# Optimization experiments

Hardware: AMD Instinct MI355X
Metric: run time of the kernel (lower is better)

The kernel has to match this reference:

```python
import jax, jax.numpy as jnp
import numpy as np

EPS = 1e-06
K = 16  # instance ids 1..K
W_IOU, W_VAR, W_SEED = 1.0, 10.0, 1.0


def _lovasz_hinge_flat(logits, labels):
    # logits, labels: (N,) flat; labels in {0,1}
    signs = 2.0 * labels - 1.0
    errors = 1.0 - logits * signs
    perm = jnp.argsort(-errors)  # descending
    errors_sorted = errors[perm]
    gt_sorted = labels[perm]
    gts = gt_sorted.sum()
    intersection = gts - jnp.cumsum(gt_sorted)
    union = gts + jnp.cumsum(1.0 - gt_sorted)
    jaccard = 1.0 - intersection / jnp.maximum(union, 1e-08)
    jaccard = jnp.concatenate([jaccard[:1], jaccard[1:] - jaccard[:-1]])
    return jnp.dot(jax.nn.relu(errors_sorted), jaccard)


def _forward(y_pred, y_true):
    B, C, H, W = y_pred.shape
    D = 2
    off = y_pred[:, :D]              # (B,D,H,W)
    sig = y_pred[:, D:2 * D]         # (B,D,H,W)
    seed = y_pred[:, 2 * D]          # (B,H,W)
    dt = y_pred.dtype

    gy, gx = jnp.meshgrid(jnp.arange(H, dtype=dt), jnp.arange(W, dtype=dt), indexing='ij')
    grid = jnp.stack([gy, gx])       # (D,H,W)
    emb = grid[None] + off           # (B,D,H,W)

    ids = jnp.arange(1, K + 1)
    mask = (y_true[:, None] == ids[None, :, None, None]).astype(dt)  # (B,K,H,W)
    count = mask.sum((2, 3))                                         # (B,K)
    safe = jnp.maximum(count, 1.0)
    present = (count > 0).astype(dt)
    n_present = jnp.maximum(present.sum(), 1.0)

    # per-instance embedding centers
    Ck = jnp.einsum('bkhw,bdhw->bkd', mask, emb) / safe[..., None]   # (B,K,D)
    sb = jnp.maximum(sig, EPS)                                       # (B,D,H,W)
    diff = emb[:, None] - Ck[..., None, None]                        # (B,K,D,H,W)
    quad = diff * diff / (2.0 * sb[:, None] ** 2)
    phi = jnp.clip(jnp.exp(-quad.sum(2)), EPS, 1.0 - EPS)            # (B,K,H,W)
    logits = jnp.log(phi) - jnp.log1p(-phi)

    lov = jax.vmap(_lovasz_hinge_flat)(logits.reshape(B * K, -1), mask.reshape(B * K, -1))
    L_iou = (lov * present.reshape(-1)).sum() / n_present

    # sigma smoothness: mean over instances of mean_{d,pixels in mask}|sig - mean_k(sig)|
    mean_sig = jnp.einsum('bkhw,bdhw->bkd', mask, sig) / safe[..., None]  # (B,K,D)
    dev = (jnp.abs(sig[:, None] - mean_sig[..., None, None]) * mask[:, :, None]).sum((2, 3, 4))
    dev = dev / (D * safe)                                           # (B,K)
    L_var = (dev * present).sum() / n_present

    seed_target = (phi * mask).sum(1)                                # (B,H,W)
    L_seed = jnp.mean((seed - seed_target) ** 2)

    return W_IOU * L_iou + W_VAR * L_var + W_SEED * L_seed


def setup_inputs() -> dict:
    key = jax.random.key(0)
    k1, k2 = jax.random.split(key)
    B, H, W = 4, 768, 768
    y_pred = jax.random.uniform(k1, (B, 5, H, W), dtype=jnp.float32)
    y_true = jax.random.randint(k2, (B, H, W), 0, K + 1)
    return {"y_pred": y_pred, "y_true": y_true}


def reference(y_pred, y_true):
    return _forward(y_pred, y_true)
```

## Files before the change

### kernel.cpp

```cpp
#include <hip/hip_runtime.h>

#define HWPIX 589824
#define Wdim 768
#define Bdim 4
#define Kdim 16
#define NBINS 2048
#define RANGE_F 16.0f
#define BIN_W (RANGE_F / NBINS)
#define INV_BIN_W (NBINS / RANGE_F)
#define EPSf 1e-6f
#define QCLIP 13.8155106f

#define NSB 192
#define Q4 (HWPIX / 4)
#define GPI (NSB * 256)
#define NTHREADS_TOT (NSB * Bdim * 256)

#define ACC_OFF 0
#define CK_OFF 320
#define MSW_OFF 448
#define NPRES_OFF 720
#define LOVARR_OFF 724
#define HIST_OFF_F 1024
#define NHIST (Bdim * Kdim * 2 * NBINS)
#define POSNH_OFF_F (HIST_OFF_F + NHIST)
#define SPART_OFF (POSNH_OFF_F + 64)
#define MPART_OFF (SPART_OFF + Bdim * NSB * 80)

__global__ __launch_bounds__(256, 3) void k_stats(const float* __restrict__ yp,
                                                  const int* __restrict__ yt,
                                                  float* __restrict__ ws,
                                                  unsigned* __restrict__ hist) {
    int b = blockIdx.y;
    int lane = threadIdx.x & 63;
    int wv = threadIdx.x >> 6;
    __shared__ float lpart[4][80];

    {
        int gtid = (blockIdx.y * NSB + blockIdx.x) * 256 + threadIdx.x;
        for (int i = gtid; i < NHIST + 64; i += NTHREADS_TOT) hist[i] = 0u;
    }

    const float4* bp4 = (const float4*)(yp + (size_t)b * 5 * HWPIX);
    const int4* bt4 = (const int4*)(yt + (size_t)b * HWPIX);

    float acc[80];
#pragma unroll
    for (int v = 0; v < 80; ++v) acc[v] = 0.f;

    for (int p = 0; p < 3; ++p) {
        int g = p * GPI + blockIdx.x * 256 + threadIdx.x;
        float4 voy = bp4[g];
        float4 vox = bp4[g + Q4];
        float4 vsy = bp4[g + 2 * Q4];
        float4 vsx = bp4[g + 3 * Q4];
        int4 vt = bt4[g];
        int hwb = g * 4;
        float oy[4] = {voy.x, voy.y, voy.z, voy.w};
        float ox[4] = {vox.x, vox.y, vox.z, vox.w};
        float sy[4] = {vsy.x, vsy.y, vsy.z, vsy.w};
        float sx[4] = {vsx.x, vsx.y, vsx.z, vsx.w};
        int tt[4] = {vt.x, vt.y, vt.z, vt.w};
#pragma unroll
        for (int j = 0; j < 4; ++j) {
            int hw = hwb + j;
            int h = hw / Wdim;
            int w = hw - h * Wdim;
            int own = tt[j] - 1;
            float vy = (float)h + oy[j];
            float vx = (float)w + ox[j];
#pragma unroll
            for (int k = 0; k < Kdim; ++k) {
                float m = (own == k) ? 1.0f : 0.0f;
                acc[k * 5 + 0] += m;
                acc[k * 5 + 1] = fmaf(m, vy, acc[k * 5 + 1]);
                acc[k * 5 + 2] = fmaf(m, vx, acc[k * 5 + 2]);
                acc[k * 5 + 3] = fmaf(m, sy[j], acc[k * 5 + 3]);
                acc[k * 5 + 4] = fmaf(m, sx[j], acc[k * 5 + 4]);
            }
        }
    }

    bool lo = (lane < 32);
#pragma unroll
    for (int v = 0; v < 40; ++v) {
        float send = lo ? acc[v + 40] : acc[v];
        float got = __shfl_xor(send, 32);
        acc[v] += lo ? got : 0.f;
        acc[v + 40] += lo ? 0.f : got;
    }
#pragma unroll
    for (int v = 0; v < 40; ++v) {
        float x = lo ? acc[v] : acc[v + 40];
#pragma unroll
        for (int o = 16; o >= 1; o >>= 1) x += __shfl_xor(x, o);
        if ((lane & 31) == 0) lpart[wv][lo ? v : v + 40] = x;
    }
    __syncthreads();
    if (threadIdx.x < 80) {
        float v = lpart[0][threadIdx.x] + lpart[1][threadIdx.x] +
                  lpart[2][threadIdx.x] + lpart[3][threadIdx.x];
        ws[SPART_OFF + (size_t)(b * NSB + blockIdx.x) * 80 + threadIdx.x] = v;
    }
}

__global__ void k_centers(float* __restrict__ ws) {
    int t = threadIdx.x;
    int b = t / 80, idx = t - b * 80;
    float s = 0.f;
    const float* sp = ws + SPART_OFF + (size_t)b * NSB * 80 + idx;
    for (int j = 0; j < NSB; ++j) s += sp[j * 80];
    ws[ACC_OFF + t] = s;
    __syncthreads();
    if (t < 64) {
        float cnt = ws[ACC_OFF + t * 5];
        float safe = fmaxf(cnt, 1.0f);
        ws[CK_OFF + t * 2 + 0] = ws[ACC_OFF + t * 5 + 1] / safe;
        ws[CK_OFF + t * 2 + 1] = ws[ACC_OFF + t * 5 + 2] / safe;
        int bb = t >> 4, kk = t & 15;
        float* mw = ws + MSW_OFF + (size_t)(bb * 17 + kk) * 4;
        mw[0] = ws[ACC_OFF + t * 5 + 3] / safe;
        mw[1] = ws[ACC_OFF + t * 5 + 4] / safe;
        mw[2] = (cnt > 0.f) ? 0.5f / cnt : 0.f;
        mw[3] = 0.f;
    }
    if (t >= 64 && t < 68) {
        float* mw = ws + MSW_OFF + (size_t)((t - 64) * 17 + 16) * 4;
        mw[0] = mw[1] = mw[2] = mw[3] = 0.f;
    }
    __syncthreads();
    if (t == 0) {
        float s2 = 0.f;
        for (int j = 0; j < 64; ++j) s2 += (ws[ACC_OFF + j * 5] > 0.f) ? 1.f : 0.f;
        ws[NPRES_OFF] = fmaxf(s2, 1.0f);
    }
}

__global__ __launch_bounds__(256, 3) void k_main(const float* __restrict__ yp,
                                                 const int* __restrict__ yt,
                                                 float* __restrict__ ws,
                                                 unsigned* __restrict__ hist) {
    int b = blockIdx.y;
    int lane = threadIdx.x & 63;
    int wv = threadIdx.x >> 6;
    __shared__ float ck_s[32];
    __shared__ float4 msw_s[17];
    __shared__ float part[4][2];
    if (threadIdx.x < 32) ck_s[threadIdx.x] = ws[CK_OFF + b * 32 + threadIdx.x];
    if (threadIdx.x < 17)
        msw_s[threadIdx.x] = ((const float4*)(ws + MSW_OFF))[b * 17 + threadIdx.x];
    __syncthreads();

    float cky[Kdim], ckx[Kdim];
#pragma unroll
    for (int k = 0; k < Kdim; ++k) {
        cky[k] = ck_s[k * 2];
        ckx[k] = ck_s[k * 2 + 1];
    }

    unsigned* hb = hist + (size_t)(b * Kdim) * 2 * NBINS;
    unsigned* posnh = hist + (size_t)NHIST;
    const float4* bp4 = (const float4*)(yp + (size_t)b * 5 * HWPIX);
    const int4* bt4 = (const int4*)(yt + (size_t)b * HWPIX);

    float varsum = 0.f, ssum = 0.f;
    for (int p = 0; p < 3; ++p) {
        int g = p * GPI + blockIdx.x * 256 + threadIdx.x;
        float4 voy = bp4[g];
        float4 vox = bp4[g + Q4];
        float4 vsy = bp4[g + 2 * Q4];
        float4 vsx = bp4[g + 3 * Q4];
        float4 vse = bp4[g + 4 * Q4];
        int4 vt = bt4[g];
        int hwb = g * 4;
        float oy[4] = {voy.x, voy.y, voy.z, voy.w};
        float ox[4] = {vox.x, vox.y, vox.z, vox.w};
        float sya[4] = {vsy.x, vsy.y, vsy.z, vsy.w};
        float sxa[4] = {vsx.x, vsx.y, vsx.z, vsx.w};
        float sea[4] = {vse.x, vse.y, vse.z, vse.w};
        int tt[4] = {vt.x, vt.y, vt.z, vt.w};
#pragma unroll
        for (int j = 0; j < 4; ++j) {
            int hw = hwb + j;
            int h = hw / Wdim;
            int w = hw - h * Wdim;
            int own = tt[j] - 1;
            float sy = sya[j], sx = sxa[j];
            float ey = (float)h + oy[j], ex = (float)w + ox[j];
            float sby = fmaxf(sy, EPSf), sbx = fmaxf(sx, EPSf);
            float iy = 0.5f / (sby * sby), ix = 0.5f / (sbx * sbx);

            unsigned sm = 0;
#pragma unroll
            for (int k = 0; k < Kdim; ++k) {
                float dy = ey - cky[k];
                float dx = ex - ckx[k];
                float q = fmaf(dy * dy, iy, dx * dx * ix);
                if (q < QCLIP) sm |= (1u << k);
            }
            int ow = (own >= 0) ? own : 16;
            float4 mw = msw_s[ow];
            float devv = fabsf(sy - mw.x) + fabsf(sx - mw.y);
            varsum = fmaf(devv, mw.z, varsum);

            float st = (own >= 0) ? EPSf : 0.f;
            while (sm) {
                int k = __ffs(sm) - 1;
                sm &= sm - 1;
                float dy = ey - ck_s[k * 2];
                float dx = ex - ck_s[k * 2 + 1];
                float q = fmaf(dy * dy, iy, dx * dx * ix);
                float phi = expf(-q);
                phi = fminf(fmaxf(phi, EPSf), 1.0f - EPSf);
                float lg = logf(phi) - log1pf(-phi);
                bool isPos = (k == own);
                float e;
                if (isPos) {
                    st = phi;
                    atomicAdd(&posnh[b * Kdim + k], 1u);
                    e = 1.0f - lg;
                } else {
                    e = 1.0f + lg;
                }
                if (e > 0.f) {
                    int bin = (int)(e * INV_BIN_W);
                    if (bin > NBINS - 1) bin = NBINS - 1;
                    atomicAdd(&hb[(k * 2 + (isPos ? 1 : 0)) * NBINS + bin], 1u);
                }
            }
            float dd = sea[j] - st;
            ssum = fmaf(dd, dd, ssum);
        }
    }
#pragma unroll
    for (int o = 32; o >= 1; o >>= 1) {
        varsum += __shfl_xor(varsum, o);
        ssum += __shfl_xor(ssum, o);
    }
    if (lane == 0) {
        part[wv][0] = varsum;
        part[wv][1] = ssum;
    }
    __syncthreads();
    if (threadIdx.x < 2) {
        float v = part[0][threadIdx.x] + part[1][threadIdx.x] +
                  part[2][threadIdx.x] + part[3][threadIdx.x];
        ws[MPART_OFF + (size_t)(b * NSB + blockIdx.x) * 2 + threadIdx.x] = v;
    }
}

__global__ void k_lovasz(float* __restrict__ ws, const unsigned* __restrict__ hist) {
    int i = blockIdx.x;
    int lane = threadIdx.x;
    float P = ws[ACC_OFF + i * 5];
    if (P < 0.5f) {
        if (lane == 0) ws[LOVARR_OFF + i] = 0.f;
        return;
    }
    const unsigned* hn = hist + (size_t)i * 2 * NBINS;
    const unsigned* hp = hn + NBINS;
    const unsigned* posnh = hist + (size_t)NHIST;
    const float C_LO = logf(EPSf) - log1pf(-EPSf);
    const int HOTBIN = (int)((1.0f - C_LO) * INV_BIN_W);
    int deficit = (int)(P + 0.5f) - (int)posnh[i];
    int carry_p = 0, carry_n = 0;
    float Jtop = 0.f;
    float trap = 0.f;
    for (int c = NBINS / 64 - 1; c >= 0; --c) {
        int m = c * 64 + lane;
        int vp = (int)hp[m];
        int vn = (int)hn[m];
        if (m == HOTBIN) vp += deficit;
        for (int o = 1; o < 64; o <<= 1) {
            int tp = __shfl_down(vp, o);
            int tn = __shfl_down(vn, o);
            if (lane + o < 64) { vp += tp; vn += tn; }
        }
        float p_edge = (float)(carry_p + vp);
        float n_edge = (float)(carry_n + vn);
        float J = 1.0f - (P - p_edge) / (P + n_edge);
        float Jn = __shfl_down(J, 1);
        if (lane == 63) Jn = Jtop;
        trap += 0.5f * (J + Jn);
        carry_p += __shfl(vp, 0);
        carry_n += __shfl(vn, 0);
        Jtop = __shfl(J, 0);
    }
    for (int o = 1; o < 64; o <<= 1) {
        float t2 = __shfl_down(trap, o);
        if (lane + o < 64) trap += t2;
    }
    if (lane == 0) ws[LOVARR_OFF + i] = trap * BIN_W;
}

__global__ void k_final(const float* __restrict__ ws, float* __restrict__ out) {
    __shared__ float r0[256], r1[256], r2[256];
    int t = threadIdx.x;
    float v = 0.f, s = 0.f, l = 0.f;
    for (int j = t; j < Bdim * NSB; j += 256) {
        v += ws[MPART_OFF + 2 * j];
        s += ws[MPART_OFF + 2 * j + 1];
    }
    if (t < 64) l = ws[LOVARR_OFF + t];
    r0[t] = v; r1[t] = s; r2[t] = l;
    __syncthreads();
    for (int o = 128; o > 0; o >>= 1) {
        if (t < o) { r0[t] += r0[t + o]; r1[t] += r1[t + o]; r2[t] += r2[t + o]; }
        __syncthreads();
    }
    if (t == 0) {
        float npres = ws[NPRES_OFF];
        out[0] = r2[0] / npres + 10.0f * (r0[0] / npres) +
                 r1[0] / (float)((size_t)Bdim * HWPIX);
    }
}

extern "C" void kernel_launch(void* const* d_in, const int* in_sizes, int n_in,
                              void* d_out, int out_size, void* d_ws, size_t ws_size,
                              hipStream_t stream) {
    const float* yp = (const float*)d_in[0];
    const int* yt = (const int*)d_in[1];
    float* ws = (float*)d_ws;
    unsigned* hist = (unsigned*)((char*)d_ws + HIST_OFF_F * 4);

    dim3 g(NSB, Bdim);
    k_stats<<<g, 256, 0, stream>>>(yp, yt, ws, hist);
    k_centers<<<1, 320, 0, stream>>>(ws);
    k_main<<<g, 256, 0, stream>>>(yp, yt, ws, hist);
    k_lovasz<<<64, 64, 0, stream>>>(ws, hist);
    k_final<<<1, 256, 0, stream>>>(ws, (float*)d_out);
}
```

Measured before the change: 87.15 us.

## Parallelize center reduction, pack FP32 math, and regrid main kernel

The single-block center reduction becomes an 80-block kernel where each wave reduces one accumulator across the 192 partials with shuffles. Computing the centers and sigma means moves into k_main's prologue, and the present count moves into k_final. The per-class accumulation in k_stats and the distance test in k_main are written with 2-wide float vectors so the compiler can emit packed FP32 instructions. k_main now uses 288 blocks of 2 passes each with launch_bounds occupancy 4. The risks are added register pressure and redundant per-block center computation.

Result: faster. 83.26 us (-4.5%).

```diff
diff --git a/kernel.cpp b/kernel.cpp
--- a/kernel.cpp
+++ b/kernel.cpp
@@ -1,4 +1,6 @@
 #include <hip/hip_runtime.h>
+
+typedef float f32x2 __attribute__((ext_vector_type(2)));
 
 #define HWPIX 589824
 #define Wdim 768
@@ -11,21 +13,21 @@
 #define EPSf 1e-6f
 #define QCLIP 13.8155106f
 
-#define NSB 192
 #define Q4 (HWPIX / 4)
-#define GPI (NSB * 256)
-#define NTHREADS_TOT (NSB * Bdim * 256)
+
+#define NSB_S 192
+#define GPI_S (NSB_S * 256)
+#define NTHREADS_S (NSB_S * Bdim * 256)
+#define NSB_M 288
+#define GPI_M (NSB_M * 256)
 
 #define ACC_OFF 0
-#define CK_OFF 320
-#define MSW_OFF 448
-#define NPRES_OFF 720
 #define LOVARR_OFF 724
 #define HIST_OFF_F 1024
 #define NHIST (Bdim * Kdim * 2 * NBINS)
 #define POSNH_OFF_F (HIST_OFF_F + NHIST)
 #define SPART_OFF (POSNH_OFF_F + 64)
-#define MPART_OFF (SPART_OFF + Bdim * NSB * 80)
+#define MPART_OFF (SPART_OFF + Bdim * NSB_S * 80)
 
 __global__ __launch_bounds__(256, 3) void k_stats(const float* __restrict__ yp,
                                                   const int* __restrict__ yt,
@@ -37,19 +39,19 @@
     __shared__ float lpart[4][80];
 
     {
-        int gtid = (blockIdx.y * NSB + blockIdx.x) * 256 + threadIdx.x;
-        for (int i = gtid; i < NHIST + 64; i += NTHREADS_TOT) hist[i] = 0u;
+        int gtid = (blockIdx.y * NSB_S + blockIdx.x) * 256 + threadIdx.x;
+        for (int i = gtid; i < NHIST + 64; i += NTHREADS_S) hist[i] = 0u;
     }
 
     const float4* bp4 = (const float4*)(yp + (size_t)b * 5 * HWPIX);
     const int4* bt4 = (const int4*)(yt + (size_t)b * HWPIX);
 
-    float acc[80];
-#pragma unroll
-    for (int v = 0; v < 80; ++v) acc[v] = 0.f;
+    f32x2 acc2[40];
+#pragma unroll
+    for (int v = 0; v < 40; ++v) acc2[v] = (f32x2){0.f, 0.f};
 
     for (int p = 0; p < 3; ++p) {
-        int g = p * GPI + blockIdx.x * 256 + threadIdx.x;
+        int g = p * GPI_S + blockIdx.x * 256 + threadIdx.x;
         float4 voy = bp4[g];
         float4 vox = bp4[g + Q4];
         float4 vsy = bp4[g + 2 * Q4];
@@ -70,28 +72,31 @@
             float vy = (float)h + oy[j];
             float vx = (float)w + ox[j];
 #pragma unroll
-            for (int k = 0; k < Kdim; ++k) {
-                float m = (own == k) ? 1.0f : 0.0f;
-                acc[k * 5 + 0] += m;
-                acc[k * 5 + 1] = fmaf(m, vy, acc[k * 5 + 1]);
-                acc[k * 5 + 2] = fmaf(m, vx, acc[k * 5 + 2]);
-                acc[k * 5 + 3] = fmaf(m, sy[j], acc[k * 5 + 3]);
-                acc[k * 5 + 4] = fmaf(m, sx[j], acc[k * 5 + 4]);
+            for (int q = 0; q < 8; ++q) {
+                f32x2 m2 = {(own == 2 * q) ? 1.0f : 0.0f,
+                            (own == 2 * q + 1) ? 1.0f : 0.0f};
+                acc2[q * 5 + 0] += m2;
+                acc2[q * 5 + 1] += m2 * vy;
+                acc2[q * 5 + 2] += m2 * vx;
+                acc2[q * 5 + 3] += m2 * sy[j];
+                acc2[q * 5 + 4] += m2 * sx[j];
             }
         }
     }
 
+#define ACCV(v) (acc2[((v) / 5 / 2) * 5 + (v) % 5][((v) / 5) & 1])
+
     bool lo = (lane < 32);
 #pragma unroll
     for (int v = 0; v < 40; ++v) {
-        float send = lo ? acc[v + 40] : acc[v];
+        float send = lo ? ACCV(v + 40) : ACCV(v);
         float got = __shfl_xor(send, 32);
-        acc[v] += lo ? got : 0.f;
-        acc[v + 40] += lo ? 0.f : got;
+        ACCV(v) += lo ? got : 0.f;
+        ACCV(v + 40) += lo ? 0.f : got;
     }
 #pragma unroll
     for (int v = 0; v < 40; ++v) {
-        float x = lo ? acc[v] : acc[v + 40];
+        float x = lo ? ACCV(v) : ACCV(v + 40);
 #pragma unroll
         for (int o = 16; o >= 1; o >>= 1) x += __shfl_xor(x, o);
         if ((lane & 31) == 0) lpart[wv][lo ? v : v + 40] = x;
@@ -100,43 +105,25 @@
     if (threadIdx.x < 80) {
         float v = lpart[0][threadIdx.x] + lpart[1][threadIdx.x] +
                   lpart[2][threadIdx.x] + lpart[3][threadIdx.x];
-        ws[SPART_OFF + (size_t)(b * NSB + blockIdx.x) * 80 + threadIdx.x] = v;
-    }
-}
-
-__global__ void k_centers(float* __restrict__ ws) {
-    int t = threadIdx.x;
-    int b = t / 80, idx = t - b * 80;
-    float s = 0.f;
-    const float* sp = ws + SPART_OFF + (size_t)b * NSB * 80 + idx;
-    for (int j = 0; j < NSB; ++j) s += sp[j * 80];
-    ws[ACC_OFF + t] = s;
-    __syncthreads();
-    if (t < 64) {
-        float cnt = ws[ACC_OFF + t * 5];
-        float safe = fmaxf(cnt, 1.0f);
-        ws[CK_OFF + t * 2 + 0] = ws[ACC_OFF + t * 5 + 1] / safe;
-        ws[CK_OFF + t * 2 + 1] = ws[ACC_OFF + t * 5 + 2] / safe;
-        int bb = t >> 4, kk = t & 15;
-        float* mw = ws + MSW_OFF + (size_t)(bb * 17 + kk) * 4;
-        mw[0] = ws[ACC_OFF + t * 5 + 3] / safe;
-        mw[1] = ws[ACC_OFF + t * 5 + 4] / safe;
-        mw[2] = (cnt > 0.f) ? 0.5f / cnt : 0.f;
-        mw[3] = 0.f;
-    }
-    if (t >= 64 && t < 68) {
-        float* mw = ws + MSW_OFF + (size_t)((t - 64) * 17 + 16) * 4;
-        mw[0] = mw[1] = mw[2] = mw[3] = 0.f;
-    }
-    __syncthreads();
-    if (t == 0) {
-        float s2 = 0.f;
-        for (int j = 0; j < 64; ++j) s2 += (ws[ACC_OFF + j * 5] > 0.f) ? 1.f : 0.f;
-        ws[NPRES_OFF] = fmaxf(s2, 1.0f);
-    }
-}
-
-__global__ __launch_bounds__(256, 3) void k_main(const float* __restrict__ yp,
+        ws[SPART_OFF + (size_t)(b * NSB_S + blockIdx.x) * 80 + threadIdx.x] = v;
+    }
+#undef ACCV
+}
+
+__global__ void k_centers2(float* __restrict__ ws) {
+    int wv = threadIdx.x >> 6;
+    int lane = threadIdx.x & 63;
+    int gw = blockIdx.x * 4 + wv;
+    int b = gw / 80, idx = gw - b * 80;
+    const float* sp = ws + SPART_OFF + (size_t)b * NSB_S * 80 + idx;
+    float x = sp[(size_t)lane * 80] + sp[(size_t)(lane + 64) * 80] +
+              sp[(size_t)(lane + 128) * 80];
+#pragma unroll
+    for (int o = 32; o >= 1; o >>= 1) x += __shfl_xor(x, o);
+    if (lane == 0) ws[ACC_OFF + b * 80 + idx] = x;
+}
+
+__global__ __launch_bounds__(256, 4) void k_main(const float* __restrict__ yp,
                                                  const int* __restrict__ yt,
                                                  float* __restrict__ ws,
                                                  unsigned* __restrict__ hist) {
@@ -146,16 +133,29 @@
     __shared__ float ck_s[32];
     __shared__ float4 msw_s[17];
     __shared__ float part[4][2];
-    if (threadIdx.x < 32) ck_s[threadIdx.x] = ws[CK_OFF + b * 32 + threadIdx.x];
-    if (threadIdx.x < 17)
-        msw_s[threadIdx.x] = ((const float4*)(ws + MSW_OFF))[b * 17 + threadIdx.x];
+    if (threadIdx.x < 16) {
+        int k = threadIdx.x;
+        const float* a = ws + ACC_OFF + (size_t)b * 80 + k * 5;
+        float cnt = a[0];
+        float safe = fmaxf(cnt, 1.0f);
+        float inv = 1.0f / safe;
+        ck_s[k * 2 + 0] = a[1] * inv;
+        ck_s[k * 2 + 1] = a[2] * inv;
+        float4 mw;
+        mw.x = a[3] * inv;
+        mw.y = a[4] * inv;
+        mw.z = (cnt > 0.f) ? 0.5f / cnt : 0.f;
+        mw.w = 0.f;
+        msw_s[k] = mw;
+    }
+    if (threadIdx.x == 16) msw_s[16] = (float4){0.f, 0.f, 0.f, 0.f};
     __syncthreads();
 
-    float cky[Kdim], ckx[Kdim];
-#pragma unroll
-    for (int k = 0; k < Kdim; ++k) {
-        cky[k] = ck_s[k * 2];
-        ckx[k] = ck_s[k * 2 + 1];
+    f32x2 cky2[8], ckx2[8];
+#pragma unroll
+    for (int q = 0; q < 8; ++q) {
+        cky2[q] = (f32x2){ck_s[4 * q], ck_s[4 * q + 2]};
+        ckx2[q] = (f32x2){ck_s[4 * q + 1], ck_s[4 * q + 3]};
     }
 
     unsigned* hb = hist + (size_t)(b * Kdim) * 2 * NBINS;
@@ -164,8 +164,8 @@
     const int4* bt4 = (const int4*)(yt + (size_t)b * HWPIX);
 
     float varsum = 0.f, ssum = 0.f;
-    for (int p = 0; p < 3; ++p) {
-        int g = p * GPI + blockIdx.x * 256 + threadIdx.x;
+    for (int p = 0; p < 2; ++p) {
+        int g = p * GPI_M + blockIdx.x * 256 + threadIdx.x;
         float4 voy = bp4[g];
         float4 vox = bp4[g + Q4];
         float4 vsy = bp4[g + 2 * Q4];
@@ -192,11 +192,12 @@
 
             unsigned sm = 0;
 #pragma unroll
-            for (int k = 0; k < Kdim; ++k) {
-                float dy = ey - cky[k];
-                float dx = ex - ckx[k];
-                float q = fmaf(dy * dy, iy, dx * dx * ix);
-                if (q < QCLIP) sm |= (1u << k);
+            for (int q = 0; q < 8; ++q) {
+                f32x2 dy2 = ey - cky2[q];
+                f32x2 dx2 = ex - ckx2[q];
+                f32x2 q2 = dy2 * dy2 * iy + dx2 * dx2 * ix;
+                if (q2.x < QCLIP) sm |= (1u << (2 * q));
+                if (q2.y < QCLIP) sm |= (1u << (2 * q + 1));
             }
             int ow = (own >= 0) ? own : 16;
             float4 mw = msw_s[ow];
@@ -245,7 +246,7 @@
     if (threadIdx.x < 2) {
         float v = part[0][threadIdx.x] + part[1][threadIdx.x] +
                   part[2][threadIdx.x] + part[3][threadIdx.x];
-        ws[MPART_OFF + (size_t)(b * NSB + blockIdx.x) * 2 + threadIdx.x] = v;
+        ws[MPART_OFF + (size_t)(b * NSB_M + blockIdx.x) * 2 + threadIdx.x] = v;
     }
 }
 
@@ -294,22 +295,28 @@
 }
 
 __global__ void k_final(const float* __restrict__ ws, float* __restrict__ out) {
-    __shared__ float r0[256], r1[256], r2[256];
+    __shared__ float r0[256], r1[256], r2[256], r3[256];
     int t = threadIdx.x;
-    float v = 0.f, s = 0.f, l = 0.f;
-    for (int j = t; j < Bdim * NSB; j += 256) {
+    float v = 0.f, s = 0.f, l = 0.f, pr = 0.f;
+    for (int j = t; j < Bdim * NSB_M; j += 256) {
         v += ws[MPART_OFF + 2 * j];
         s += ws[MPART_OFF + 2 * j + 1];
     }
-    if (t < 64) l = ws[LOVARR_OFF + t];
-    r0[t] = v; r1[t] = s; r2[t] = l;
+    if (t < 64) {
+        l = ws[LOVARR_OFF + t];
+        pr = (ws[ACC_OFF + t * 5] > 0.f) ? 1.f : 0.f;
+    }
+    r0[t] = v; r1[t] = s; r2[t] = l; r3[t] = pr;
     __syncthreads();
     for (int o = 128; o > 0; o >>= 1) {
-        if (t < o) { r0[t] += r0[t + o]; r1[t] += r1[t + o]; r2[t] += r2[t + o]; }
+        if (t < o) {
+            r0[t] += r0[t + o]; r1[t] += r1[t + o];
+            r2[t] += r2[t + o]; r3[t] += r3[t + o];
+        }
         __syncthreads();
     }
     if (t == 0) {
-        float npres = ws[NPRES_OFF];
+        float npres = fmaxf(r3[0], 1.0f);
         out[0] = r2[0] / npres + 10.0f * (r0[0] / npres) +
                  r1[0] / (float)((size_t)Bdim * HWPIX);
     }
@@ -323,10 +330,11 @@
     float* ws = (float*)d_ws;
     unsigned* hist = (unsigned*)((char*)d_ws + HIST_OFF_F * 4);
 
-    dim3 g(NSB, Bdim);
-    k_stats<<<g, 256, 0, stream>>>(yp, yt, ws, hist);
-    k_centers<<<1, 320, 0, stream>>>(ws);
-    k_main<<<g, 256, 0, stream>>>(yp, yt, ws, hist);
+    dim3 gs(NSB_S, Bdim);
+    dim3 gm(NSB_M, Bdim);
+    k_stats<<<gs, 256, 0, stream>>>(yp, yt, ws, hist);
+    k_centers2<<<80, 256, 0, stream>>>(ws);
+    k_main<<<gm, 256, 0, stream>>>(yp, yt, ws, hist);
     k_lovasz<<<64, 64, 0, stream>>>(ws, hist);
     k_final<<<1, 256, 0, stream>>>(ws, (float*)d_out);
 }
```
